# Kernel tuning notes

Hardware: AMD Instinct MI355X
Metric: run time of the kernel (lower is better)

Reference implementation:

```python
import jax, jax.numpy as jnp
import numpy as np

B, N, C = 4, 4096, 1024
NUM_HEADS = 16
HEAD_DIM = C // NUM_HEADS


def setup_inputs() -> dict:
    key = jax.random.key(0)
    k1, k2, k3, k4 = jax.random.split(key, 4)
    s_in = 1.0 / np.sqrt(C)
    return {
        "x": jax.random.normal(k1, (B, N, C), dtype=jnp.float32),
        "H": 64,
        "W": 64,
        "Wqkv": jax.random.normal(k2, (3 * C, C), dtype=jnp.float32) * s_in,
        "Wproj": jax.random.normal(k3, (C, C), dtype=jnp.float32) * s_in,
        "bproj": jnp.zeros((C,), dtype=jnp.float32),
        "alpha": jnp.ones((NUM_HEADS,), dtype=jnp.float32),
    }


def reference(x, H, W, Wqkv, Wproj, bproj, alpha):
    Bb, Nn, Cc = x.shape
    h, d = NUM_HEADS, HEAD_DIM
    # qkv: [B, N, 3C] -> [3, B, h, N, d]
    qkv = jnp.einsum('bnc,oc->bno', x, Wqkv)
    qkv = qkv.reshape(Bb, Nn, 3, h, d).transpose(2, 0, 3, 1, 4)
    q, k, v = qkv[0], qkv[1], qkv[2]  # each [B, h, N, d]
    # channel attention: contract over tokens N -> [B, h, d, d]
    attn = jnp.einsum('bhnd,bhne->bhde', k, q) / alpha[None, :, None, None]
    attn = jax.nn.softmax(attn, axis=-1)
    # (dropout is identity in eval/reference mode)
    # head_out: [B, h, d, N] -> transpose -> [B, N, h, d] -> concat heads
    out = jnp.einsum('bhde,bhne->bhdn', attn, v)
    out = out.transpose(0, 3, 1, 2).reshape(Bb, Nn, Cc)
    return jnp.einsum('bnc,oc->bno', out, Wproj) + bproj
```

## Files before the change

### kernel.cpp

```cpp
#include <hip/hip_runtime.h>
#include <hip/hip_bf16.h>
#include <cstdint>
#include <cstddef>

typedef unsigned short u16;
typedef __bf16 bf16x8 __attribute__((ext_vector_type(8)));
typedef float f32x4 __attribute__((ext_vector_type(4)));
typedef unsigned short u16x4 __attribute__((ext_vector_type(4)));

#define AS1(p) ((__attribute__((address_space(1))) void*)(p))
#define AS3(p) ((__attribute__((address_space(3))) void*)(p))

__device__ __forceinline__ float bf2f(u16 u) {
  unsigned v = ((unsigned)u) << 16; float f; __builtin_memcpy(&f, &v, 4); return f;
}
__device__ __forceinline__ u16 f2bf(float f) {
  unsigned u; __builtin_memcpy(&u, &f, 4);
  u += 0x7FFFu + ((u >> 16) & 1u);
  return (u16)(u >> 16);
}

__global__ __launch_bounds__(256) void convert_kernel(const float* __restrict__ src,
                                                      u16* __restrict__ dst, int n4) {
  int i = blockIdx.x * blockDim.x + threadIdx.x;
  int stride = gridDim.x * blockDim.x;
  for (; i < n4; i += stride) {
    float4 v = ((const float4*)src)[i];
    u16x4 o;
    o.x = f2bf(v.x); o.y = f2bf(v.y); o.z = f2bf(v.z); o.w = f2bf(v.w);
    ((u16x4*)dst)[i] = o;
  }
}

__global__ __launch_bounds__(256) void convert_split_kernel(const float* __restrict__ src,
                                                            u16* __restrict__ hi,
                                                            u16* __restrict__ lo, int n4) {
  int i = blockIdx.x * blockDim.x + threadIdx.x;
  int stride = gridDim.x * blockDim.x;
  for (; i < n4; i += stride) {
    float4 v = ((const float4*)src)[i];
    u16x4 oh, ol;
    oh.x = f2bf(v.x); ol.x = f2bf(v.x - bf2f(oh.x));
    oh.y = f2bf(v.y); ol.y = f2bf(v.y - bf2f(oh.y));
    oh.z = f2bf(v.z); ol.z = f2bf(v.z - bf2f(oh.z));
    oh.w = f2bf(v.w); ol.w = f2bf(v.w - bf2f(oh.w));
    ((u16x4*)hi)[i] = oh;
    ((u16x4*)lo)[i] = ol;
  }
}

__global__ __launch_bounds__(256) void transpose_split_kernel(const float* __restrict__ x,
                                                              u16* __restrict__ Xb,
                                                              u16* __restrict__ XThi,
                                                              u16* __restrict__ XTlo) {
  __shared__ u16 lhi[64 * 68];
  __shared__ u16 llo[64 * 68];
  const int t  = threadIdx.x;
  const int nT = blockIdx.x, cT = blockIdx.y, b = blockIdx.z;
  const size_t xbase = ((size_t)b * 4096 + nT * 64) * 1024 + cT * 64;
  const int c4 = (t & 15) * 4;
  const int r0 = t >> 4;
#pragma unroll
  for (int j = 0; j < 4; ++j) {
    int r = r0 + j * 16;
    float4 v = *(const float4*)(x + xbase + (size_t)r * 1024 + c4);
    u16x4 hi;
    hi.x = f2bf(v.x); hi.y = f2bf(v.y); hi.z = f2bf(v.z); hi.w = f2bf(v.w);
    *(u16x4*)(Xb + xbase + (size_t)r * 1024 + c4) = hi;
    u16 lo[4];
    lo[0] = f2bf(v.x - bf2f(hi.x)); lo[1] = f2bf(v.y - bf2f(hi.y));
    lo[2] = f2bf(v.z - bf2f(hi.z)); lo[3] = f2bf(v.w - bf2f(hi.w));
    u16 hia[4] = { hi.x, hi.y, hi.z, hi.w };
#pragma unroll
    for (int i = 0; i < 4; ++i) {
      lhi[(c4 + i) * 68 + r] = hia[i];
      llo[(c4 + i) * 68 + r] = lo[i];
    }
  }
  __syncthreads();
  const int c  = t >> 2;
  const int n0 = (t & 3) * 16;
  const size_t tbase = ((size_t)b * 1024 + cT * 64 + c) * 4096 + nT * 64 + n0;
#pragma unroll
  for (int q = 0; q < 4; ++q) {
    *(u16x4*)(XThi + tbase + q * 4) = *(const u16x4*)(lhi + c * 68 + n0 + q * 4);
    *(u16x4*)(XTlo + tbase + q * 4) = *(const u16x4*)(llo + c * 68 + n0 + q * 4);
  }
}

template<bool OUT_BF16, bool HAS_BIAS>
__global__ __launch_bounds__(256) void gemm_bt(const u16* __restrict__ A,
                                               const u16* __restrict__ B,
                                               void* __restrict__ Cv,
                                               const float* __restrict__ bias,
                                               int M, int N, int K) {
  __shared__ __align__(16) u16 lA[128 * 32];
  __shared__ __align__(16) u16 lB[128 * 32];
  const int tid  = threadIdx.x;
  const int lane = tid & 63;
  const int wave = tid >> 6;
  const int rowTile = blockIdx.x * 128;
  const int colTile = blockIdx.y * 128;
  const int wr = (wave >> 1) * 64;
  const int wc = (wave & 1) * 64;

  f32x4 acc[4][4] = {};
  const int m  = lane & 15;
  const int ko = (lane >> 4) * 8;

  for (int kt = 0; kt < K; kt += 32) {
#pragma unroll
    for (int i = 0; i < 2; ++i) {
      int idx = i * 256 + tid;
      int row = idx >> 2;
      int kc  = (idx & 3) * 8;
      int ldsOff = (i * 256 + (tid & 192)) * 16;
      __builtin_amdgcn_global_load_lds(AS1(A + (size_t)(rowTile + row) * K + kt + kc),
                                       AS3((char*)lA + ldsOff), 16, 0, 0);
      __builtin_amdgcn_global_load_lds(AS1(B + (size_t)(colTile + row) * K + kt + kc),
                                       AS3((char*)lB + ldsOff), 16, 0, 0);
    }
    __syncthreads();
    bf16x8 af[4], bfr[4];
#pragma unroll
    for (int rb = 0; rb < 4; ++rb)
      af[rb] = *(const bf16x8*)(lA + (wr + rb * 16 + m) * 32 + ko);
#pragma unroll
    for (int cb = 0; cb < 4; ++cb)
      bfr[cb] = *(const bf16x8*)(lB + (wc + cb * 16 + m) * 32 + ko);
#pragma unroll
    for (int rb = 0; rb < 4; ++rb)
#pragma unroll
      for (int cb = 0; cb < 4; ++cb)
        acc[rb][cb] = __builtin_amdgcn_mfma_f32_16x16x32_bf16(af[rb], bfr[cb], acc[rb][cb], 0, 0, 0);
    __syncthreads();
  }

  const int crow0 = rowTile + wr + (lane >> 4) * 4;
  const int ccol0 = colTile + wc + (lane & 15);
#pragma unroll
  for (int rb = 0; rb < 4; ++rb) {
#pragma unroll
    for (int cb = 0; cb < 4; ++cb) {
      int col = ccol0 + cb * 16;
      float bv = HAS_BIAS ? bias[col] : 0.f;
#pragma unroll
      for (int r = 0; r < 4; ++r) {
        int row = crow0 + rb * 16 + r;
        float v = acc[rb][cb][r] + bv;
        if (OUT_BF16) ((u16*)Cv)[(size_t)row * N + col] = f2bf(v);
        else          ((float*)Cv)[(size_t)row * N + col] = v;
      }
    }
  }
}

__global__ __launch_bounds__(256) void gemm_vm(const u16* __restrict__ V,
                                               const u16* __restrict__ Mb,
                                               float* __restrict__ Y,
                                               const float* __restrict__ bias) {
  __shared__ __align__(16) u16 lA[128 * 32];
  __shared__ __align__(16) u16 lB[128 * 32];
  const int tid  = threadIdx.x;
  const int lane = tid & 63;
  const int wave = tid >> 6;
  const int rowTile = blockIdx.x * 128;
  const int colTile = blockIdx.y * 128;
  const int bz = blockIdx.z;
  const u16* A = V + ((size_t)bz << 22);
  const u16* B = Mb + ((size_t)bz << 20);
  float* C = Y + ((size_t)bz << 22);
  const int wr = (wave >> 1) * 64;
  const int wc = (wave & 1) * 64;

  f32x4 acc[4][4] = {};
  const int m  = lane & 15;
  const int ko = (lane >> 4) * 8;

  for (int kt = 0; kt < 1024; kt += 32) {
#pragma unroll
    for (int i = 0; i < 2; ++i) {
      int idx = i * 256 + tid;
      int row = idx >> 2;
      int kc  = (idx & 3) * 8;
      int ldsOff = (i * 256 + (tid & 192)) * 16;
      __builtin_amdgcn_global_load_lds(AS1(A + (size_t)(rowTile + row) * 1024 + kt + kc),
                                       AS3((char*)lA + ldsOff), 16, 0, 0);
      __builtin_amdgcn_global_load_lds(AS1(B + (size_t)(colTile + row) * 1024 + kt + kc),
                                       AS3((char*)lB + ldsOff), 16, 0, 0);
    }
    __syncthreads();
    bf16x8 af[4], bfr[4];
#pragma unroll
    for (int rb = 0; rb < 4; ++rb)
      af[rb] = *(const bf16x8*)(lA + (wr + rb * 16 + m) * 32 + ko);
#pragma unroll
    for (int cb = 0; cb < 4; ++cb)
      bfr[cb] = *(const bf16x8*)(lB + (wc + cb * 16 + m) * 32 + ko);
#pragma unroll
    for (int rb = 0; rb < 4; ++rb)
#pragma unroll
      for (int cb = 0; cb < 4; ++cb)
        acc[rb][cb] = __builtin_amdgcn_mfma_f32_16x16x32_bf16(af[rb], bfr[cb], acc[rb][cb], 0, 0, 0);
    __syncthreads();
  }

  const int crow0 = rowTile + wr + (lane >> 4) * 4;
  const int ccol0 = colTile + wc + (lane & 15);
#pragma unroll
  for (int rb = 0; rb < 4; ++rb)
#pragma unroll
    for (int cb = 0; cb < 4; ++cb) {
      int col = ccol0 + cb * 16;
      float bv = bias[col];
#pragma unroll
      for (int r = 0; r < 4; ++r)
        C[(size_t)(crow0 + rb * 16 + r) * 1024 + col] = acc[rb][cb][r] + bv;
    }
}

__global__ __launch_bounds__(256) void gemm_gram(const u16* __restrict__ XThi,
                                                 const u16* __restrict__ XTlo,
                                                 float* __restrict__ Gpart) {
  __shared__ __align__(16) u16 lAh[128 * 32];
  __shared__ __align__(16) u16 lAl[128 * 32];
  __shared__ __align__(16) u16 lBh[128 * 32];
  __shared__ __align__(16) u16 lBl[128 * 32];
  const int tid  = threadIdx.x;
  const int lane = tid & 63;
  const int wave = tid >> 6;
  const int wr = (wave >> 1) * 64;
  const int wc = (wave & 1) * 64;
  const int m  = lane & 15;
  const int ko = (lane >> 4) * 8;

  const int jx = blockIdx.x;
  const int b  = blockIdx.y;
  const int tile = jx >> 2, kq = jx & 3;
  int t = tile, rt = 0;
  while (t >= 8 - rt) { t -= 8 - rt; ++rt; }
  const int ct = rt + t;
  const bool diag = (rt == ct);
  int rT = rt, cT = ct;
  if (!diag && kq >= 2) { rT = ct; cT = rt; }
  const int slice = kq & 1;
  const int rowTile = rT * 128, colTile = cT * 128;
  const int k0 = kq * 1024;

  const u16* Ahp = XThi + ((size_t)b << 22);
  const u16* Alp = XTlo + ((size_t)b << 22);

  f32x4 acc[4][4] = {};
  for (int kt = k0; kt < k0 + 1024; kt += 32) {
#pragma unroll
    for (int i = 0; i < 2; ++i) {
      int idx = i * 256 + tid;
      int row = idx >> 2;
      int kc  = (idx & 3) * 8;
      int ldsOff = (i * 256 + (tid & 192)) * 16;
      size_t aoff = (size_t)(rowTile + row) * 4096 + kt + kc;
      size_t boff = (size_t)(colTile + row) * 4096 + kt + kc;
      __builtin_amdgcn_global_load_lds(AS1(Ahp + aoff), AS3((char*)lAh + ldsOff), 16, 0, 0);
      __builtin_amdgcn_global_load_lds(AS1(Alp + aoff), AS3((char*)lAl + ldsOff), 16, 0, 0);
      __builtin_amdgcn_global_load_lds(AS1(Ahp + boff), AS3((char*)lBh + ldsOff), 16, 0, 0);
      __builtin_amdgcn_global_load_lds(AS1(Alp + boff), AS3((char*)lBl + ldsOff), 16, 0, 0);
    }
    __syncthreads();
    bf16x8 ah[4], al[4], bh[4], bl[4];
#pragma unroll
    for (int rb = 0; rb < 4; ++rb) {
      ah[rb] = *(const bf16x8*)(lAh + (wr + rb * 16 + m) * 32 + ko);
      al[rb] = *(const bf16x8*)(lAl + (wr + rb * 16 + m) * 32 + ko);
    }
#pragma unroll
    for (int cb = 0; cb < 4; ++cb) {
      bh[cb] = *(const bf16x8*)(lBh + (wc + cb * 16 + m) * 32 + ko);
      bl[cb] = *(const bf16x8*)(lBl + (wc + cb * 16 + m) * 32 + ko);
    }
#pragma unroll
    for (int rb = 0; rb < 4; ++rb)
#pragma unroll
      for (int cb = 0; cb < 4; ++cb) {
        acc[rb][cb] = __builtin_amdgcn_mfma_f32_16x16x32_bf16(ah[rb], bh[cb], acc[rb][cb], 0, 0, 0);
        acc[rb][cb] = __builtin_amdgcn_mfma_f32_16x16x32_bf16(ah[rb], bl[cb], acc[rb][cb], 0, 0, 0);
        acc[rb][cb] = __builtin_amdgcn_mfma_f32_16x16x32_bf16(al[rb], bh[cb], acc[rb][cb], 0, 0, 0);
      }
    __syncthreads();
  }

  float* out = Gpart + ((size_t)(slice * 4 + b) << 20);
  const int crow0 = rowTile + wr + (lane >> 4) * 4;
  const int ccol0 = colTile + wc + (lane & 15);
  if (diag) {
#pragma unroll
    for (int rb = 0; rb < 4; ++rb)
#pragma unroll
      for (int cb = 0; cb < 4; ++cb)
#pragma unroll
        for (int r = 0; r < 4; ++r)
          atomicAdd(&out[(size_t)(crow0 + rb * 16 + r) * 1024 + ccol0 + cb * 16],
                    acc[rb][cb][r]);
  } else {
#pragma unroll
    for (int rb = 0; rb < 4; ++rb)
#pragma unroll
      for (int cb = 0; cb < 4; ++cb)
#pragma unroll
        for (int r = 0; r < 4; ++r)
          out[(size_t)(crow0 + rb * 16 + r) * 1024 + ccol0 + cb * 16] = acc[rb][cb][r];
  }
}

__global__ __launch_bounds__(256) void gram_reduce_split(const float* __restrict__ Gp,
                                                         u16* __restrict__ Ghi,
                                                         u16* __restrict__ Glo) {
  const int rt = blockIdx.x, ct = blockIdx.y, b = blockIdx.z;
  const bool diag128 = (rt >> 1) == (ct >> 1);
  const float* s0 = Gp + ((size_t)b << 20);
  const float* s1 = Gp + ((size_t)(4 + b) << 20);
  __shared__ float lT[64 * 68];
  const int t = threadIdx.x;
  const int r = t >> 2;
  const int c16 = (t & 3) * 16;

  if (!diag128) {
    const size_t bb = (size_t)(ct * 64 + r) * 1024 + rt * 64 + c16;
#pragma unroll
    for (int q = 0; q < 4; ++q) {
      float4 v0 = *(const float4*)(s0 + bb + q * 4);
      float4 v1 = *(const float4*)(s1 + bb + q * 4);
      float4 s = { v0.x + v1.x, v0.y + v1.y, v0.z + v1.z, v0.w + v1.w };
      *(float4*)(lT + r * 68 + c16 + q * 4) = s;
    }
    __syncthreads();
  }

  const size_t ab = (size_t)(rt * 64 + r) * 1024 + ct * 64 + c16;
  const size_t ob = ((size_t)b << 20) + ab;
#pragma unroll
  for (int q = 0; q < 4; ++q) {
    float4 v0 = *(const float4*)(s0 + ab + q * 4);
    float4 v1 = *(const float4*)(s1 + ab + q * 4);
    float g[4] = { v0.x + v1.x, v0.y + v1.y, v0.z + v1.z, v0.w + v1.w };
    if (!diag128) {
#pragma unroll
      for (int i = 0; i < 4; ++i) g[i] += lT[(c16 + q * 4 + i) * 68 + r];
    }
    u16x4 oh, ol;
    oh.x = f2bf(g[0]); ol.x = f2bf(g[0] - bf2f(oh.x));
    oh.y = f2bf(g[1]); ol.y = f2bf(g[1] - bf2f(oh.y));
    oh.z = f2bf(g[2]); ol.z = f2bf(g[2] - bf2f(oh.z));
    oh.w = f2bf(g[3]); ol.w = f2bf(g[3] - bf2f(oh.w));
    *(u16x4*)(Ghi + ob + q * 4) = oh;
    *(u16x4*)(Glo + ob + q * 4) = ol;
  }
}

__global__ __launch_bounds__(256) void gemm_tprime(const u16* __restrict__ Wqh,
                                                   const u16* __restrict__ Wql,
                                                   const u16* __restrict__ Ghi,
                                                   const u16* __restrict__ Glo,
                                                   u16* __restrict__ Tph,
                                                   u16* __restrict__ Tpl) {
  __shared__ __align__(16) u16 lAh[128 * 32];
  __shared__ __align__(16) u16 lAl[128 * 32];
  __shared__ __align__(16) u16 lBh[128 * 32];
  __shared__ __align__(16) u16 lBl[128 * 32];
  const int tid  = threadIdx.x;
  const int lane = tid & 63;
  const int wave = tid >> 6;
  const int rowTile = blockIdx.x * 128;
  const int colTile = blockIdx.y * 128;
  const size_t zoff = (size_t)blockIdx.z << 20;
  const int wr = (wave >> 1) * 64;
  const int wc = (wave & 1) * 64;

  f32x4 acc[4][4] = {};
  const int m  = lane & 15;
  const int ko = (lane >> 4) * 8;

  for (int kt = 0; kt < 1024; kt += 32) {
#pragma unroll
    for (int i = 0; i < 2; ++i) {
      int idx = i * 256 + tid;
      int row = idx >> 2;
      int kc  = (idx & 3) * 8;
      int ldsOff = (i * 256 + (tid & 192)) * 16;
      size_t aoff = (size_t)(rowTile + row) * 1024 + kt + kc;
      size_t boff = zoff + (size_t)(colTile + row) * 1024 + kt + kc;
      __builtin_amdgcn_global_load_lds(AS1(Wqh + aoff), AS3((char*)lAh + ldsOff), 16, 0, 0);
      __builtin_amdgcn_global_load_lds(AS1(Wql + aoff), AS3((char*)lAl + ldsOff), 16, 0, 0);
      __builtin_amdgcn_global_load_lds(AS1(Ghi + boff), AS3((char*)lBh + ldsOff), 16, 0, 0);
      __builtin_amdgcn_global_load_lds(AS1(Glo + boff), AS3((char*)lBl + ldsOff), 16, 0, 0);
    }
    __syncthreads();
    bf16x8 ah[4], al[4], bh[4], bl[4];
#pragma unroll
    for (int rb = 0; rb < 4; ++rb) {
      ah[rb] = *(const bf16x8*)(lAh + (wr + rb * 16 + m) * 32 + ko);
      al[rb] = *(const bf16x8*)(lAl + (wr + rb * 16 + m) * 32 + ko);
    }
#pragma unroll
    for (int cb = 0; cb < 4; ++cb) {
      bh[cb] = *(const bf16x8*)(lBh + (wc + cb * 16 + m) * 32 + ko);
      bl[cb] = *(const bf16x8*)(lBl + (wc + cb * 16 + m) * 32 + ko);
    }
#pragma unroll
    for (int rb = 0; rb < 4; ++rb)
#pragma unroll
      for (int cb = 0; cb < 4; ++cb) {
        acc[rb][cb] = __builtin_amdgcn_mfma_f32_16x16x32_bf16(ah[rb], bh[cb], acc[rb][cb], 0, 0, 0);
        acc[rb][cb] = __builtin_amdgcn_mfma_f32_16x16x32_bf16(ah[rb], bl[cb], acc[rb][cb], 0, 0, 0);
        acc[rb][cb] = __builtin_amdgcn_mfma_f32_16x16x32_bf16(al[rb], bh[cb], acc[rb][cb], 0, 0, 0);
      }
    __syncthreads();
  }

  const int crow0 = rowTile + wr + (lane >> 4) * 4;
  const int ccol0 = colTile + wc + (lane & 15);
#pragma unroll
  for (int rb = 0; rb < 4; ++rb)
#pragma unroll
    for (int cb = 0; cb < 4; ++cb)
#pragma unroll
      for (int r = 0; r < 4; ++r) {
        float v = acc[rb][cb][r];
        u16 hi = f2bf(v);
        u16 lo = f2bf(v - bf2f(hi));
        size_t off = zoff + (size_t)(crow0 + rb * 16 + r) * 1024 + ccol0 + cb * 16;
        Tph[off] = hi;
        Tpl[off] = lo;
      }
}

__global__ __launch_bounds__(256) void s_softmax_kernel(const u16* __restrict__ Wqh,
                                                        const u16* __restrict__ Wql,
                                                        const u16* __restrict__ Tph,
                                                        const u16* __restrict__ Tpl,
                                                        const float* __restrict__ alpha,
                                                        u16* __restrict__ attnT) {
  const int h = blockIdx.x, b = blockIdx.y;
  const int tid = threadIdx.x, lane = tid & 63, wave = tid >> 6;
  __shared__ __align__(16) u16 lAh[64 * 32];
  __shared__ __align__(16) u16 lAl[64 * 32];
  __shared__ __align__(16) u16 lBh[64 * 32];
  __shared__ __align__(16) u16 lBl[64 * 32];

  const size_t aBase = (size_t)(1024 + h * 64) * 1024;
  const size_t bBase = ((size_t)b << 20) + (size_t)(h * 64) * 1024;

  f32x4 acc[4] = {};
  const int m  = lane & 15;
  const int ko = (lane >> 4) * 8;
  const int srow = tid >> 2;
  const int skc  = (tid & 3) * 8;
  const int ldsOff = (tid & 192) * 16;

  for (int kt = 0; kt < 1024; kt += 32) {
    __builtin_amdgcn_global_load_lds(AS1(Wqh + aBase + (size_t)srow * 1024 + kt + skc),
                                     AS3((char*)lAh + ldsOff), 16, 0, 0);
    __builtin_amdgcn_global_load_lds(AS1(Wql + aBase + (size_t)srow * 1024 + kt + skc),
                                     AS3((char*)lAl + ldsOff), 16, 0, 0);
    __builtin_amdgcn_global_load_lds(AS1(Tph + bBase + (size_t)srow * 1024 + kt + skc),
                                     AS3((char*)lBh + ldsOff), 16, 0, 0);
    __builtin_amdgcn_global_load_lds(AS1(Tpl + bBase + (size_t)srow * 1024 + kt + skc),
                                     AS3((char*)lBl + ldsOff), 16, 0, 0);
    __syncthreads();
    bf16x8 ah = *(const bf16x8*)(lAh + (wave * 16 + m) * 32 + ko);
    bf16x8 al = *(const bf16x8*)(lAl + (wave * 16 + m) * 32 + ko);
#pragma unroll
    for (int cb = 0; cb < 4; ++cb) {
      bf16x8 bh = *(const bf16x8*)(lBh + (cb * 16 + m) * 32 + ko);
      bf16x8 bl = *(const bf16x8*)(lBl + (cb * 16 + m) * 32 + ko);
      acc[cb] = __builtin_amdgcn_mfma_f32_16x16x32_bf16(ah, bh, acc[cb], 0, 0, 0);
      acc[cb] = __builtin_amdgcn_mfma_f32_16x16x32_bf16(ah, bl, acc[cb], 0, 0, 0);
      acc[cb] = __builtin_amdgcn_mfma_f32_16x16x32_bf16(al, bh, acc[cb], 0, 0, 0);
    }
    __syncthreads();
  }

  const float invA = 1.f / alpha[h];
  const int g = lane >> 4;
  const size_t obase = (size_t)(b * 16 + h) * 4096;
#pragma unroll
  for (int r = 0; r < 4; ++r) {
    int d = wave * 16 + g * 4 + r;
    float s[4];
#pragma unroll
    for (int cb = 0; cb < 4; ++cb) s[cb] = acc[cb][r] * invA;
    float mx = fmaxf(fmaxf(s[0], s[1]), fmaxf(s[2], s[3]));
#pragma unroll
    for (int o = 1; o < 16; o <<= 1) mx = fmaxf(mx, __shfl_xor(mx, o, 64));
    float e[4]; float sum = 0.f;
#pragma unroll
    for (int cb = 0; cb < 4; ++cb) { e[cb] = __expf(s[cb] - mx); sum += e[cb]; }
#pragma unroll
    for (int o = 1; o < 16; o <<= 1) sum += __shfl_xor(sum, o, 64);
    float inv = 1.f / sum;
#pragma unroll
    for (int cb = 0; cb < 4; ++cb) {
      int e_idx = cb * 16 + (lane & 15);
      attnT[obase + (size_t)e_idx * 64 + d] = f2bf(e[cb] * inv);
    }
  }
}

__global__ __launch_bounds__(256) void m_build_kernel(const u16* __restrict__ Wpb,
                                                      const u16* __restrict__ attnT,
                                                      u16* __restrict__ Mb) {
  const int oT = blockIdx.x, h = blockIdx.y, b = blockIdx.z;
  const int tid = threadIdx.x, lane = tid & 63, wave = tid >> 6;
  __shared__ __align__(16) u16 lA[128 * 64];
  __shared__ __align__(16) u16 lB[64 * 64];
  const int bh = b * 16 + h;
#pragma unroll
  for (int i = 0; i < 4; ++i) {
    int idx = i * 256 + tid;
    int row = idx >> 3;
    int kc  = (idx & 7) * 8;
    int ldsOff = (i * 256 + (tid & 192)) * 16;
    __builtin_amdgcn_global_load_lds(AS1(Wpb + (size_t)(oT * 128 + row) * 1024 + h * 64 + kc),
                                     AS3((char*)lA + ldsOff), 16, 0, 0);
  }
#pragma unroll
  for (int i = 0; i < 2; ++i) {
    int idx = i * 256 + tid;
    int ldsOff = (i * 256 + (tid & 192)) * 16;
    __builtin_amdgcn_global_load_lds(AS1(attnT + (size_t)bh * 4096 + idx * 8),
                                     AS3((char*)lB + ldsOff), 16, 0, 0);
  }
  __syncthreads();
  const int m  = lane & 15;
  const int ko = (lane >> 4) * 8;
  const int wr = wave * 32;
  f32x4 acc[2][4] = {};
#pragma unroll
  for (int ks = 0; ks < 2; ++ks) {
#pragma unroll
    for (int rb = 0; rb < 2; ++rb) {
      bf16x8 a = *(const bf16x8*)(lA + (wr + rb * 16 + m) * 64 + ks * 32 + ko);
#pragma unroll
      for (int cb = 0; cb < 4; ++cb) {
        bf16x8 bb = *(const bf16x8*)(lB + (cb * 16 + m) * 64 + ks * 32 + ko);
        acc[rb][cb] = __builtin_amdgcn_mfma_f32_16x16x32_bf16(a, bb, acc[rb][cb], 0, 0, 0);
      }
    }
  }
  u16* out = Mb + ((size_t)b << 20);
#pragma unroll
  for (int rb = 0; rb < 2; ++rb)
#pragma unroll
    for (int cb = 0; cb < 4; ++cb) {
      int col = h * 64 + cb * 16 + (lane & 15);
#pragma unroll
      for (int r = 0; r < 4; ++r) {
        int row = oT * 128 + wr + rb * 16 + (lane >> 4) * 4 + r;
        out[(size_t)row * 1024 + col] = f2bf(acc[rb][cb][r]);
      }
    }
}

extern "C" void kernel_launch(void* const* d_in, const int* in_sizes, int n_in,
                              void* d_out, int out_size, void* d_ws, size_t ws_size,
                              hipStream_t stream) {
  const float* x     = (const float*)d_in[0];
  const float* Wqkv  = (const float*)d_in[3];
  const float* Wproj = (const float*)d_in[4];
  const float* bproj = (const float*)d_in[5];
  const float* alpha = (const float*)d_in[6];

  char* ws = (char*)d_ws;
  u16*   Xb     = (u16*)ws;
  float* Gpart  = (float*)ws;
  u16*   Mb     = (u16*)ws;
  u16*   XThi   = (u16*)(ws + 33554432);
  u16*   attnTb = (u16*)(ws + 33554432);
  u16*   XTlo  = (u16*)(ws + 67108864);
  u16*   Ghi   = (u16*)(ws + 67108864);
  u16*   Glo   = (u16*)(ws + 75497472);
  u16*   Tph   = (u16*)(ws + 83886080);
  u16*   Tpl   = (u16*)(ws + 92274688);
  u16*   Wqh   = (u16*)(ws + 100663296);
  u16*   Wql   = (u16*)(ws + 106954752);
  u16*   Vb    = (u16*)(ws + 113246208);
  u16*   Wpb   = (u16*)(ws + 146800640);

  transpose_split_kernel<<<dim3(64, 16, 4), 256, 0, stream>>>(x, Xb, XThi, XTlo);
  convert_split_kernel<<<256, 256, 0, stream>>>(Wqkv, Wqh, Wql, 3145728 / 4);
  convert_kernel<<<128, 256, 0, stream>>>(Wproj, Wpb, 1048576 / 4);
  gemm_bt<true, false><<<dim3(128, 8), 256, 0, stream>>>(
      Xb, Wqh + (size_t)2048 * 1024, Vb, nullptr, 16384, 1024, 1024);
  hipMemsetAsync(Gpart, 0, (size_t)33554432, stream);
  gemm_gram<<<dim3(144, 4), 256, 0, stream>>>(XThi, XTlo, Gpart);
  gram_reduce_split<<<dim3(16, 16, 4), 256, 0, stream>>>(Gpart, Ghi, Glo);
  gemm_tprime<<<dim3(8, 8, 4), 256, 0, stream>>>(Wqh, Wql, Ghi, Glo, Tph, Tpl);
  s_softmax_kernel<<<dim3(16, 4), 256, 0, stream>>>(Wqh, Wql, Tph, Tpl, alpha, attnTb);
  m_build_kernel<<<dim3(8, 16, 4), 256, 0, stream>>>(Wpb, attnTb, Mb);
  gemm_vm<<<dim3(32, 8, 4), 256, 0, stream>>>(Vb, Mb, (float*)d_out, bproj);
}
```

Before: 441.0 us.

## Replace GEMMs with 256x256 multi-stage pipelined kernel and drop Gram atomics

Replaces the two 128x128 single-buffered bf16 GEMMs with one templated 512-thread kernel. It uses 256x256 tiles, a 4-deep LDS ring filled by async global_load_lds, swizzled LDS indexing, split barriers and raised priority around the MFMA bursts. The Gram kernel is rescheduled so diagonal tiles get whole K halves and are written directly, which removes the atomics and the memset of the partial buffer. The transpose also pads its LDS rows to 72 and uses 16-byte stores. The new GEMM uses more LDS and registers per block and launches far fewer blocks, which risks lower occupancy and poorer load balance.

```diff
diff --git a/kernel.cpp b/kernel.cpp
--- a/kernel.cpp
+++ b/kernel.cpp
@@ -7,6 +7,7 @@
 typedef __bf16 bf16x8 __attribute__((ext_vector_type(8)));
 typedef float f32x4 __attribute__((ext_vector_type(4)));
 typedef unsigned short u16x4 __attribute__((ext_vector_type(4)));
+typedef unsigned short u16x8 __attribute__((ext_vector_type(8)));
 
 #define AS1(p) ((__attribute__((address_space(1))) void*)(p))
 #define AS3(p) ((__attribute__((address_space(3))) void*)(p))
@@ -53,8 +54,8 @@
                                                               u16* __restrict__ Xb,
                                                               u16* __restrict__ XThi,
                                                               u16* __restrict__ XTlo) {
-  __shared__ u16 lhi[64 * 68];
-  __shared__ u16 llo[64 * 68];
+  __shared__ u16 lhi[64 * 72];
+  __shared__ u16 llo[64 * 72];
   const int t  = threadIdx.x;
   const int nT = blockIdx.x, cT = blockIdx.y, b = blockIdx.z;
   const size_t xbase = ((size_t)b * 4096 + nT * 64) * 1024 + cT * 64;
@@ -73,150 +74,156 @@
     u16 hia[4] = { hi.x, hi.y, hi.z, hi.w };
 #pragma unroll
     for (int i = 0; i < 4; ++i) {
-      lhi[(c4 + i) * 68 + r] = hia[i];
-      llo[(c4 + i) * 68 + r] = lo[i];
+      lhi[(c4 + i) * 72 + r] = hia[i];
+      llo[(c4 + i) * 72 + r] = lo[i];
     }
   }
   __syncthreads();
   const int c  = t >> 2;
   const int n0 = (t & 3) * 16;
   const size_t tbase = ((size_t)b * 1024 + cT * 64 + c) * 4096 + nT * 64 + n0;
-#pragma unroll
-  for (int q = 0; q < 4; ++q) {
-    *(u16x4*)(XThi + tbase + q * 4) = *(const u16x4*)(lhi + c * 68 + n0 + q * 4);
-    *(u16x4*)(XTlo + tbase + q * 4) = *(const u16x4*)(llo + c * 68 + n0 + q * 4);
-  }
+  *(u16x8*)(XThi + tbase)     = *(const u16x8*)(lhi + c * 72 + n0);
+  *(u16x8*)(XThi + tbase + 8) = *(const u16x8*)(lhi + c * 72 + n0 + 8);
+  *(u16x8*)(XTlo + tbase)     = *(const u16x8*)(llo + c * 72 + n0);
+  *(u16x8*)(XTlo + tbase + 8) = *(const u16x8*)(llo + c * 72 + n0 + 8);
 }
 
 template<bool OUT_BF16, bool HAS_BIAS>
-__global__ __launch_bounds__(256) void gemm_bt(const u16* __restrict__ A,
-                                               const u16* __restrict__ B,
-                                               void* __restrict__ Cv,
-                                               const float* __restrict__ bias,
-                                               int M, int N, int K) {
-  __shared__ __align__(16) u16 lA[128 * 32];
-  __shared__ __align__(16) u16 lB[128 * 32];
+__global__ __launch_bounds__(512, 2) void gemm_pipe(const u16* __restrict__ A,
+                                                    const u16* __restrict__ B,
+                                                    void* __restrict__ Cv,
+                                                    const float* __restrict__ bias,
+                                                    int M, int N, int K,
+                                                    size_t sA, size_t sB, size_t sC) {
+  __shared__ __align__(16) u16 lds[4][2][8192];
   const int tid  = threadIdx.x;
   const int lane = tid & 63;
   const int wave = tid >> 6;
-  const int rowTile = blockIdx.x * 128;
-  const int colTile = blockIdx.y * 128;
-  const int wr = (wave >> 1) * 64;
-  const int wc = (wave & 1) * 64;
-
-  f32x4 acc[4][4] = {};
-  const int m  = lane & 15;
-  const int ko = (lane >> 4) * 8;
-
-  for (int kt = 0; kt < K; kt += 32) {
-#pragma unroll
-    for (int i = 0; i < 2; ++i) {
-      int idx = i * 256 + tid;
-      int row = idx >> 2;
-      int kc  = (idx & 3) * 8;
-      int ldsOff = (i * 256 + (tid & 192)) * 16;
-      __builtin_amdgcn_global_load_lds(AS1(A + (size_t)(rowTile + row) * K + kt + kc),
-                                       AS3((char*)lA + ldsOff), 16, 0, 0);
-      __builtin_amdgcn_global_load_lds(AS1(B + (size_t)(colTile + row) * K + kt + kc),
-                                       AS3((char*)lB + ldsOff), 16, 0, 0);
-    }
-    __syncthreads();
-    bf16x8 af[4], bfr[4];
-#pragma unroll
-    for (int rb = 0; rb < 4; ++rb)
-      af[rb] = *(const bf16x8*)(lA + (wr + rb * 16 + m) * 32 + ko);
-#pragma unroll
-    for (int cb = 0; cb < 4; ++cb)
-      bfr[cb] = *(const bf16x8*)(lB + (wc + cb * 16 + m) * 32 + ko);
-#pragma unroll
-    for (int rb = 0; rb < 4; ++rb)
-#pragma unroll
-      for (int cb = 0; cb < 4; ++cb)
-        acc[rb][cb] = __builtin_amdgcn_mfma_f32_16x16x32_bf16(af[rb], bfr[cb], acc[rb][cb], 0, 0, 0);
-    __syncthreads();
-  }
-
-  const int crow0 = rowTile + wr + (lane >> 4) * 4;
-  const int ccol0 = colTile + wc + (lane & 15);
-#pragma unroll
-  for (int rb = 0; rb < 4; ++rb) {
-#pragma unroll
-    for (int cb = 0; cb < 4; ++cb) {
-      int col = ccol0 + cb * 16;
-      float bv = HAS_BIAS ? bias[col] : 0.f;
-#pragma unroll
-      for (int r = 0; r < 4; ++r) {
-        int row = crow0 + rb * 16 + r;
-        float v = acc[rb][cb][r] + bv;
-        if (OUT_BF16) ((u16*)Cv)[(size_t)row * N + col] = f2bf(v);
-        else          ((float*)Cv)[(size_t)row * N + col] = v;
+  const int wm = wave >> 2, wn = wave & 3;
+  const int rowTile = blockIdx.x * 256;
+  const int colTile = blockIdx.y * 256;
+  A += (size_t)blockIdx.z * sA;
+  B += (size_t)blockIdx.z * sB;
+
+  size_t srcA[2], srcB[2];
+  int ldsOff[2];
+#pragma unroll
+  for (int j = 0; j < 2; ++j) {
+    const int L = j * 512 + tid;
+    const int sr = L >> 3;
+    const int slot = (L & 7) ^ (sr & 7);
+    const int r  = (sr << 1) | (slot >> 2);
+    const int kq = slot & 3;
+    srcA[j] = (size_t)(rowTile + r) * K + kq * 8;
+    srcB[j] = (size_t)(colTile + r) * K + kq * 8;
+    ldsOff[j] = (j * 512 + (tid & 448)) * 16;
+  }
+
+  const int m15 = lane & 15, kq4 = lane >> 4;
+  const int r0a = wm * 128 + m15, sa0 = r0a >> 1;
+  const int idxA0 = sa0 * 64 + (((((r0a & 1) << 2) | kq4)) ^ (sa0 & 7)) * 8;
+  const int r0b = wn * 64 + m15, sb0 = r0b >> 1;
+  const int idxB0 = sb0 * 64 + (((((r0b & 1) << 2) | kq4)) ^ (sb0 & 7)) * 8;
+
+  const int NT = K >> 5;
+
+  auto stageA = [&](int tt) {
+    char* d = (char*)&lds[tt & 3][0][0];
+    const int kt = tt << 5;
+#pragma unroll
+    for (int j = 0; j < 2; ++j)
+      __builtin_amdgcn_global_load_lds(AS1(A + srcA[j] + kt), AS3(d + ldsOff[j]), 16, 0, 0);
+  };
+  auto stageB = [&](int tt) {
+    char* d = (char*)&lds[tt & 3][1][0];
+    const int kt = tt << 5;
+#pragma unroll
+    for (int j = 0; j < 2; ++j)
+      __builtin_amdgcn_global_load_lds(AS1(B + srcB[j] + kt), AS3(d + ldsOff[j]), 16, 0, 0);
+  };
+
+  stageA(0); stageB(0);
+  if (NT > 1) { stageA(1); stageB(1); }
+  if (NT > 2) { stageA(2); stageB(2); }
+  if (NT > 2) asm volatile("s_waitcnt vmcnt(8)" ::: "memory");
+  else        asm volatile("s_waitcnt vmcnt(0)" ::: "memory");
+  __builtin_amdgcn_sched_barrier(0);
+  __builtin_amdgcn_s_barrier();
+  __builtin_amdgcn_sched_barrier(0);
+
+  f32x4 acc[8][4] = {};
+  for (int t = 0; t < NT; ++t) {
+    const u16* bufA = &lds[t & 3][0][0];
+    const u16* bufB = &lds[t & 3][1][0];
+    bf16x8 a[8], bfr[4];
+#pragma unroll
+    for (int ni = 0; ni < 4; ++ni) bfr[ni] = *(const bf16x8*)(bufB + idxB0 + ni * 512);
+#pragma unroll
+    for (int mi = 0; mi < 4; ++mi) a[mi] = *(const bf16x8*)(bufA + idxA0 + mi * 512);
+    if (t + 3 < NT) stageA(t + 3);
+    __builtin_amdgcn_sched_barrier(0);
+    __builtin_amdgcn_s_barrier();
+    __builtin_amdgcn_sched_barrier(0);
+    __builtin_amdgcn_s_setprio(1);
+#pragma unroll
+    for (int mi = 0; mi < 4; ++mi)
+#pragma unroll
+      for (int ni = 0; ni < 4; ++ni)
+        acc[mi][ni] = __builtin_amdgcn_mfma_f32_16x16x32_bf16(a[mi], bfr[ni], acc[mi][ni], 0, 0, 0);
+    __builtin_amdgcn_s_setprio(0);
+    __builtin_amdgcn_sched_barrier(0);
+    __builtin_amdgcn_s_barrier();
+    __builtin_amdgcn_sched_barrier(0);
+#pragma unroll
+    for (int mi = 4; mi < 8; ++mi) a[mi] = *(const bf16x8*)(bufA + idxA0 + mi * 512);
+    if (t + 3 < NT) stageB(t + 3);
+    __builtin_amdgcn_sched_barrier(0);
+    __builtin_amdgcn_s_barrier();
+    __builtin_amdgcn_sched_barrier(0);
+    __builtin_amdgcn_s_setprio(1);
+#pragma unroll
+    for (int mi = 4; mi < 8; ++mi)
+#pragma unroll
+      for (int ni = 0; ni < 4; ++ni)
+        acc[mi][ni] = __builtin_amdgcn_mfma_f32_16x16x32_bf16(a[mi], bfr[ni], acc[mi][ni], 0, 0, 0);
+    __builtin_amdgcn_s_setprio(0);
+    if (t < NT - 1) {
+      if (t + 3 < NT)      asm volatile("s_waitcnt vmcnt(8)" ::: "memory");
+      else if (t + 2 < NT) asm volatile("s_waitcnt vmcnt(4)" ::: "memory");
+      else                 asm volatile("s_waitcnt vmcnt(0)" ::: "memory");
+    }
+    __builtin_amdgcn_sched_barrier(0);
+    __builtin_amdgcn_s_barrier();
+    __builtin_amdgcn_sched_barrier(0);
+  }
+
+  const int crow0 = rowTile + wm * 128 + (lane >> 4) * 4;
+  const int ccol0 = colTile + wn * 64 + m15;
+  if constexpr (OUT_BF16) {
+    u16* C = (u16*)Cv + (size_t)blockIdx.z * sC;
+#pragma unroll
+    for (int mi = 0; mi < 8; ++mi)
+#pragma unroll
+      for (int ni = 0; ni < 4; ++ni) {
+        const int col = ccol0 + ni * 16;
+        const float bv = HAS_BIAS ? bias[col] : 0.f;
+#pragma unroll
+        for (int r = 0; r < 4; ++r)
+          C[(size_t)(crow0 + mi * 16 + r) * N + col] = f2bf(acc[mi][ni][r] + bv);
       }
-    }
-  }
-}
-
-__global__ __launch_bounds__(256) void gemm_vm(const u16* __restrict__ V,
-                                               const u16* __restrict__ Mb,
-                                               float* __restrict__ Y,
-                                               const float* __restrict__ bias) {
-  __shared__ __align__(16) u16 lA[128 * 32];
-  __shared__ __align__(16) u16 lB[128 * 32];
-  const int tid  = threadIdx.x;
-  const int lane = tid & 63;
-  const int wave = tid >> 6;
-  const int rowTile = blockIdx.x * 128;
-  const int colTile = blockIdx.y * 128;
-  const int bz = blockIdx.z;
-  const u16* A = V + ((size_t)bz << 22);
-  const u16* B = Mb + ((size_t)bz << 20);
-  float* C = Y + ((size_t)bz << 22);
-  const int wr = (wave >> 1) * 64;
-  const int wc = (wave & 1) * 64;
-
-  f32x4 acc[4][4] = {};
-  const int m  = lane & 15;
-  const int ko = (lane >> 4) * 8;
-
-  for (int kt = 0; kt < 1024; kt += 32) {
-#pragma unroll
-    for (int i = 0; i < 2; ++i) {
-      int idx = i * 256 + tid;
-      int row = idx >> 2;
-      int kc  = (idx & 3) * 8;
-      int ldsOff = (i * 256 + (tid & 192)) * 16;
-      __builtin_amdgcn_global_load_lds(AS1(A + (size_t)(rowTile + row) * 1024 + kt + kc),
-                                       AS3((char*)lA + ldsOff), 16, 0, 0);
-      __builtin_amdgcn_global_load_lds(AS1(B + (size_t)(colTile + row) * 1024 + kt + kc),
-                                       AS3((char*)lB + ldsOff), 16, 0, 0);
-    }
-    __syncthreads();
-    bf16x8 af[4], bfr[4];
-#pragma unroll
-    for (int rb = 0; rb < 4; ++rb)
-      af[rb] = *(const bf16x8*)(lA + (wr + rb * 16 + m) * 32 + ko);
-#pragma unroll
-    for (int cb = 0; cb < 4; ++cb)
-      bfr[cb] = *(const bf16x8*)(lB + (wc + cb * 16 + m) * 32 + ko);
-#pragma unroll
-    for (int rb = 0; rb < 4; ++rb)
-#pragma unroll
-      for (int cb = 0; cb < 4; ++cb)
-        acc[rb][cb] = __builtin_amdgcn_mfma_f32_16x16x32_bf16(af[rb], bfr[cb], acc[rb][cb], 0, 0, 0);
-    __syncthreads();
-  }
-
-  const int crow0 = rowTile + wr + (lane >> 4) * 4;
-  const int ccol0 = colTile + wc + (lane & 15);
-#pragma unroll
-  for (int rb = 0; rb < 4; ++rb)
-#pragma unroll
-    for (int cb = 0; cb < 4; ++cb) {
-      int col = ccol0 + cb * 16;
-      float bv = bias[col];
-#pragma unroll
-      for (int r = 0; r < 4; ++r)
-        C[(size_t)(crow0 + rb * 16 + r) * 1024 + col] = acc[rb][cb][r] + bv;
-    }
+  } else {
+    float* C = (float*)Cv + (size_t)blockIdx.z * sC;
+#pragma unroll
+    for (int mi = 0; mi < 8; ++mi)
+#pragma unroll
+      for (int ni = 0; ni < 4; ++ni) {
+        const int col = ccol0 + ni * 16;
+        const float bv = HAS_BIAS ? bias[col] : 0.f;
+#pragma unroll
+        for (int r = 0; r < 4; ++r)
+          C[(size_t)(crow0 + mi * 16 + r) * N + col] = acc[mi][ni][r] + bv;
+      }
+  }
 }
 
 __global__ __launch_bounds__(256) void gemm_gram(const u16* __restrict__ XThi,
@@ -236,22 +243,29 @@
 
   const int jx = blockIdx.x;
   const int b  = blockIdx.y;
-  const int tile = jx >> 2, kq = jx & 3;
-  int t = tile, rt = 0;
-  while (t >= 8 - rt) { t -= 8 - rt; ++rt; }
-  const int ct = rt + t;
-  const bool diag = (rt == ct);
-  int rT = rt, cT = ct;
-  if (!diag && kq >= 2) { rT = ct; cT = rt; }
-  const int slice = kq & 1;
+  int rT, cT, slice, k0, kend;
+  if (jx < 112) {
+    const int tile = jx >> 2, kq = jx & 3;
+    int t = tile, rt = 0;
+    while (t >= 7 - rt) { t -= 7 - rt; ++rt; }
+    const int ct = rt + 1 + t;
+    rT = rt; cT = ct;
+    if (kq >= 2) { rT = ct; cT = rt; }
+    slice = kq & 1;
+    k0 = kq * 1024; kend = k0 + 1024;
+  } else {
+    const int j2 = jx - 112;
+    rT = cT = j2 >> 1;
+    slice = j2 & 1;
+    k0 = slice * 2048; kend = k0 + 2048;
+  }
   const int rowTile = rT * 128, colTile = cT * 128;
-  const int k0 = kq * 1024;
 
   const u16* Ahp = XThi + ((size_t)b << 22);
   const u16* Alp = XTlo + ((size_t)b << 22);
 
   f32x4 acc[4][4] = {};
-  for (int kt = k0; kt < k0 + 1024; kt += 32) {
+  for (int kt = k0; kt < kend; kt += 32) {
 #pragma unroll
     for (int i = 0; i < 2; ++i) {
       int idx = i * 256 + tid;
@@ -291,24 +305,13 @@
   float* out = Gpart + ((size_t)(slice * 4 + b) << 20);
   const int crow0 = rowTile + wr + (lane >> 4) * 4;
   const int ccol0 = colTile + wc + (lane & 15);
-  if (diag) {
-#pragma unroll
-    for (int rb = 0; rb < 4; ++rb)
-#pragma unroll
-      for (int cb = 0; cb < 4; ++cb)
-#pragma unroll
-        for (int r = 0; r < 4; ++r)
-          atomicAdd(&out[(size_t)(crow0 + rb * 16 + r) * 1024 + ccol0 + cb * 16],
-                    acc[rb][cb][r]);
-  } else {
-#pragma unroll
-    for (int rb = 0; rb < 4; ++rb)
-#pragma unroll
-      for (int cb = 0; cb < 4; ++cb)
-#pragma unroll
-        for (int r = 0; r < 4; ++r)
-          out[(size_t)(crow0 + rb * 16 + r) * 1024 + ccol0 + cb * 16] = acc[rb][cb][r];
-  }
+#pragma unroll
+  for (int rb = 0; rb < 4; ++rb)
+#pragma unroll
+    for (int cb = 0; cb < 4; ++cb)
+#pragma unroll
+      for (int r = 0; r < 4; ++r)
+        out[(size_t)(crow0 + rb * 16 + r) * 1024 + ccol0 + cb * 16] = acc[rb][cb][r];
 }
 
 __global__ __launch_bounds__(256) void gram_reduce_split(const float* __restrict__ Gp,
@@ -588,13 +591,15 @@
   transpose_split_kernel<<<dim3(64, 16, 4), 256, 0, stream>>>(x, Xb, XThi, XTlo);
   convert_split_kernel<<<256, 256, 0, stream>>>(Wqkv, Wqh, Wql, 3145728 / 4);
   convert_kernel<<<128, 256, 0, stream>>>(Wproj, Wpb, 1048576 / 4);
-  gemm_bt<true, false><<<dim3(128, 8), 256, 0, stream>>>(
-      Xb, Wqh + (size_t)2048 * 1024, Vb, nullptr, 16384, 1024, 1024);
-  hipMemsetAsync(Gpart, 0, (size_t)33554432, stream);
-  gemm_gram<<<dim3(144, 4), 256, 0, stream>>>(XThi, XTlo, Gpart);
+  gemm_pipe<true, false><<<dim3(64, 4, 1), 512, 0, stream>>>(
+      Xb, Wqh + (size_t)2048 * 1024, Vb, nullptr, 16384, 1024, 1024,
+      (size_t)0, (size_t)0, (size_t)0);
+  gemm_gram<<<dim3(128, 4), 256, 0, stream>>>(XThi, XTlo, Gpart);
   gram_reduce_split<<<dim3(16, 16, 4), 256, 0, stream>>>(Gpart, Ghi, Glo);
   gemm_tprime<<<dim3(8, 8, 4), 256, 0, stream>>>(Wqh, Wql, Ghi, Glo, Tph, Tpl);
   s_softmax_kernel<<<dim3(16, 4), 256, 0, stream>>>(Wqh, Wql, Tph, Tpl, alpha, attnTb);
   m_build_kernel<<<dim3(8, 16, 4), 256, 0, stream>>>(Wpb, attnTb, Mb);
-  gemm_vm<<<dim3(32, 8, 4), 256, 0, stream>>>(Vb, Mb, (float*)d_out, bproj);
-}
+  gemm_pipe<false, true><<<dim3(16, 4, 4), 512, 0, stream>>>(
+      Vb, Mb, (float*)d_out, bproj, 4096, 1024, 1024,
+      (size_t)1 << 22, (size_t)1 << 20, (size_t)1 << 22);
+}
```

After: 422.4 us. 1.04x faster.
